# Kernel tuning notes

Hardware: AMD Instinct MI355X
Metric: run time of the kernel (lower is better)

## Reference

```python
import jax, jax.numpy as jnp
import numpy as np
import math

E = 2048        # embed_dim
H = 16          # num_heads
HD = E // H // 2  # head_dim = 64
DEPTH = 12
LAMBDA_INIT = 0.8 - 0.6 * math.exp(-0.3 * DEPTH)


def setup_inputs() -> dict:
    key = jax.random.key(0)
    ks = jax.random.split(key, 9)
    s = 0.02
    return {
        "x": jax.random.normal(ks[0], (2, 2048, E), jnp.float32),
        "Wq": jax.random.normal(ks[1], (E, E), jnp.float32) * s,
        "Wk": jax.random.normal(ks[2], (E, E), jnp.float32) * s,  # n_rep = 1
        "Wv": jax.random.normal(ks[3], (E, E), jnp.float32) * s,
        "Wo": jax.random.normal(ks[4], (E, E), jnp.float32) * s,
        "lq1": jax.random.normal(ks[5], (HD,), jnp.float32) * 0.1,
        "lk1": jax.random.normal(ks[6], (HD,), jnp.float32) * 0.1,
        "lq2": jax.random.normal(ks[7], (HD,), jnp.float32) * 0.1,
        "lk2": jax.random.normal(ks[8], (HD,), jnp.float32) * 0.1,
    }


def reference(x, Wq, Wk, Wv, Wo, lq1, lk1, lq2, lk2):
    b, t, e = x.shape
    scaling = HD ** (-0.5)
    # projections; split into 2*H sub-heads of dim HD for q/k, H heads of 2*HD for v
    q = (x @ Wq).reshape(b, t, 2 * H, HD).transpose(0, 2, 1, 3) * scaling  # [b,2H,t,hd]
    k = (x @ Wk).reshape(b, t, 2 * H, HD).transpose(0, 2, 1, 3)           # [b,2H,t,hd]
    v = (x @ Wv).reshape(b, t, H, 2 * HD).transpose(0, 2, 1, 3)           # [b,H,t,2hd]

    scores = jnp.einsum('bhqd,bhkd->bhqk', q, k)  # [b,2H,t,t]
    causal = jnp.triu(jnp.full((t, t), -jnp.inf, dtype=jnp.float32), 1)
    aw = jax.nn.softmax((scores + causal).astype(jnp.float32), axis=-1)

    lam = (jnp.exp(jnp.sum(lq1 * lk1)) - jnp.exp(jnp.sum(lq2 * lk2)) + LAMBDA_INIT)
    aw = aw.reshape(b, H, 2, t, t)
    aw = aw[:, :, 0] - lam * aw[:, :, 1]  # differential attention

    attn = jnp.einsum('bhqk,bhkd->bhqd', aw, v)  # [b,H,t,2hd]
    # RMSNorm over last dim (no affine), eps=1e-5
    attn = attn * jax.lax.rsqrt(jnp.mean(attn * attn, axis=-1, keepdims=True) + 1e-5)
    attn = attn * (1.0 - LAMBDA_INIT)
    attn = attn.transpose(0, 2, 1, 3).reshape(b, t, H * 2 * HD)
    return attn @ Wo
```

## Files before the change

### kernel.cpp

```cpp
#include <hip/hip_runtime.h>
#include <stdint.h>

typedef __bf16 bf16_t;
typedef __bf16 bf16x8 __attribute__((ext_vector_type(8)));
typedef __bf16 bf16x4 __attribute__((ext_vector_type(4)));
typedef float  f32x4  __attribute__((ext_vector_type(4)));
typedef float  f32x16 __attribute__((ext_vector_type(16)));
typedef unsigned int u32;

#define L2E 1.44269504088896340736f
#define LAMBDA_INIT 0.7836057665316245f
#define ONE_MINUS_LAMBDA_INIT 0.2163942334683755f

__device__ __forceinline__ void gload_lds16(const void* g, void* l) {
  __builtin_amdgcn_global_load_lds(
      (const __attribute__((address_space(1))) char*)(uintptr_t)g,
      (__attribute__((address_space(3))) char*)(uintptr_t)l, 16, 0, 0);
}

__device__ __forceinline__ f32x4 mfma_bf16(bf16x8 a, bf16x8 b, f32x4 c) {
  return __builtin_amdgcn_mfma_f32_16x16x32_bf16(a, b, c, 0, 0, 0);
}
__device__ __forceinline__ f32x16 mfma32(bf16x8 a, bf16x8 b, f32x16 c) {
  return __builtin_amdgcn_mfma_f32_32x32x16_bf16(a, b, c, 0, 0, 0);
}

__device__ __forceinline__ u32 pkbf(float a, float b) {
  union { bf16_t h[2]; u32 u; } x;
  x.h[0] = (bf16_t)a; x.h[1] = (bf16_t)b;
  return x.u;
}
__device__ __forceinline__ void pl32swap(u32& a, u32& b) {
  asm volatile("v_permlane32_swap_b32 %0, %1" : "+v"(a), "+v"(b));
}

__global__ __launch_bounds__(256) void cvt_bf16(const float* __restrict__ in,
                                                bf16_t* __restrict__ out) {
  const size_t idx = ((size_t)blockIdx.x * 256 + threadIdx.x) * 8;
  float4 a = *(const float4*)(in + idx);
  float4 c = *(const float4*)(in + idx + 4);
  bf16x8 v;
  v[0] = (bf16_t)a.x; v[1] = (bf16_t)a.y; v[2] = (bf16_t)a.z; v[3] = (bf16_t)a.w;
  v[4] = (bf16_t)c.x; v[5] = (bf16_t)c.y; v[6] = (bf16_t)c.z; v[7] = (bf16_t)c.w;
  *(bf16x8*)(out + idx) = v;
}

__global__ __launch_bounds__(256) void cvt_wT(const float* __restrict__ W,
                                              bf16_t* __restrict__ WT, float scale) {
  __shared__ float t[64][65];
  const int k0 = blockIdx.x * 64, n0 = blockIdx.y * 64;
  const int r = threadIdx.x >> 2, cg = threadIdx.x & 3;
#pragma unroll
  for (int q = 0; q < 4; ++q) {
    float4 v = *(const float4*)(W + (size_t)(k0 + r) * 2048 + n0 + cg * 16 + q * 4);
    t[r][cg * 16 + q * 4 + 0] = v.x;
    t[r][cg * 16 + q * 4 + 1] = v.y;
    t[r][cg * 16 + q * 4 + 2] = v.z;
    t[r][cg * 16 + q * 4 + 3] = v.w;
  }
  __syncthreads();
  bf16x8 o0, o1;
#pragma unroll
  for (int j = 0; j < 8; ++j) o0[j] = (bf16_t)(t[cg * 16 + j][r] * scale);
#pragma unroll
  for (int j = 0; j < 8; ++j) o1[j] = (bf16_t)(t[cg * 16 + 8 + j][r] * scale);
  bf16_t* dst = WT + (size_t)(n0 + r) * 2048 + k0 + cg * 16;
  *(bf16x8*)dst = o0;
  *(bf16x8*)(dst + 8) = o1;
}

__global__ void lam_kernel(const float* lq1, const float* lk1,
                           const float* lq2, const float* lk2, float* out) {
  const int l = threadIdx.x;
  float p1 = lq1[l] * lk1[l];
  float p2 = lq2[l] * lk2[l];
#pragma unroll
  for (int d = 1; d < 64; d <<= 1) {
    p1 += __shfl_xor(p1, d);
    p2 += __shfl_xor(p2, d);
  }
  if (l == 0) *out = expf(p1) - expf(p2) + LAMBDA_INIT;
}

template <int OUTMODE>
__global__ __launch_bounds__(256, 2) void gemm_bt(const bf16_t* __restrict__ A,
                                                  const bf16_t* __restrict__ Bt,
                                                  void* __restrict__ Cv) {
  __shared__ __align__(16) bf16_t As[128 * 64];
  __shared__ __align__(16) bf16_t Bs[128 * 64];
  const int tid = threadIdx.x;
  const int w = tid >> 6, lane = tid & 63;
  const int wr = w >> 1, wc = w & 1;
  const int lm = lane >> 4, ln = lane & 15;
  const int flat = (int)blockIdx.y * (int)gridDim.x + (int)blockIdx.x;
  const int swz = (flat & 7) * 64 + (flat >> 3);
  const int m0 = (swz & 31) * 128, n0 = (swz >> 5) * 128;

  const f32x4 vzero = {0.f, 0.f, 0.f, 0.f};
  f32x4 acc[4][4];
#pragma unroll
  for (int m = 0; m < 4; ++m)
#pragma unroll
    for (int n = 0; n < 4; ++n) acc[m][n] = vzero;

  for (int k0 = 0; k0 < 2048; k0 += 64) {
    __syncthreads();
#pragma unroll
    for (int j = 0; j < 4; ++j) {
      const int inst = w * 4 + j;
      const int row = inst * 8 + (lane >> 3);
      const int cb = ((lane & 7) * 16) ^ ((row & 7) << 4);
      gload_lds16(A + (size_t)(m0 + row) * 2048 + k0 + (cb >> 1),
                  (char*)As + inst * 1024);
      gload_lds16(Bt + (size_t)(n0 + row) * 2048 + k0 + (cb >> 1),
                  (char*)Bs + inst * 1024);
    }
    asm volatile("s_waitcnt vmcnt(0)" ::: "memory");
    __syncthreads();

#pragma unroll
    for (int kc = 0; kc < 2; ++kc) {
      bf16x8 af[4], bfr[4];
#pragma unroll
      for (int m = 0; m < 4; ++m) {
        const int row = wr * 64 + m * 16 + ln;
        int off = row * 128 + kc * 64 + lm * 16;
        off ^= (row & 7) << 4;
        af[m] = *(const bf16x8*)((const char*)As + off);
      }
#pragma unroll
      for (int n = 0; n < 4; ++n) {
        const int row = wc * 64 + n * 16 + ln;
        int off = row * 128 + kc * 64 + lm * 16;
        off ^= (row & 7) << 4;
        bfr[n] = *(const bf16x8*)((const char*)Bs + off);
      }
      __builtin_amdgcn_s_setprio(1);
#pragma unroll
      for (int m = 0; m < 4; ++m)
#pragma unroll
        for (int n = 0; n < 4; ++n) acc[m][n] = mfma_bf16(af[m], bfr[n], acc[m][n]);
      __builtin_amdgcn_s_setprio(0);
    }
  }

  if (OUTMODE == 0) {
    bf16_t* C = (bf16_t*)Cv;
#pragma unroll
    for (int m = 0; m < 4; ++m)
#pragma unroll
      for (int n = 0; n < 4; ++n)
#pragma unroll
        for (int r = 0; r < 4; ++r) {
          const size_t grow = m0 + wr * 64 + m * 16 + lm * 4 + r;
          const int gcol = n0 + wc * 64 + n * 16 + ln;
          C[grow * 2048 + gcol] = (bf16_t)acc[m][n][r];
        }
  } else if (OUTMODE == 1) {
    bf16_t* C = (bf16_t*)Cv;
#pragma unroll
    for (int m = 0; m < 4; ++m)
#pragma unroll
      for (int n = 0; n < 4; ++n) {
        const size_t gcol = n0 + wc * 64 + n * 16 + ln;
        const int growb = m0 + wr * 64 + m * 16 + lm * 4;
        bf16x4 v;
#pragma unroll
        for (int r = 0; r < 4; ++r) v[r] = (bf16_t)acc[m][n][r];
        *(bf16x4*)(C + gcol * 4096 + growb) = v;
      }
  } else {
    float* C = (float*)Cv;
#pragma unroll
    for (int m = 0; m < 4; ++m)
#pragma unroll
      for (int n = 0; n < 4; ++n)
#pragma unroll
        for (int r = 0; r < 4; ++r) {
          const size_t grow = m0 + wr * 64 + m * 16 + lm * 4 + r;
          const int gcol = n0 + wc * 64 + n * 16 + ln;
          C[grow * 2048 + gcol] = acc[m][n][r];
        }
  }
}

__global__ __launch_bounds__(256, 2) void flash_diff(const bf16_t* __restrict__ Q,
                                                     const bf16_t* __restrict__ K,
                                                     const bf16_t* __restrict__ Vt,
                                                     bf16_t* __restrict__ attnb,
                                                     const float* __restrict__ lamP) {
  __shared__ __align__(16) char smem[81920];

  const int tid = threadIdx.x;
  const int w = tid >> 6, lane = tid & 63;
  const int qh = w >> 1, s = w & 1;
  const int l31 = lane & 31, hi = lane >> 5;
  const int h = blockIdx.y, b = blockIdx.z;
  const size_t bt0 = (size_t)b * 2048;
  const float lam = *lamP;

  auto stage_kv = [&](int buf, int k0) {
#pragma unroll
    for (int j = 0; j < 4; ++j) {
      const int inst = w * 4 + j;
      {
        const int row = inst * 4 + (lane >> 4);
        const int cb = ((lane & 15) * 16) ^ ((row & 7) << 4);
        gload_lds16(K + (bt0 + k0 + row) * 2048 + h * 128 + (cb >> 1),
                    smem + 16384 + buf * 16384 + inst * 1024);
      }
      {
        const int row = inst * 8 + (lane >> 3);
        const int cb = ((lane & 7) * 16) ^ ((row & 7) << 4);
        gload_lds16(Vt + (size_t)(h * 128 + row) * 4096 + bt0 + k0 + (cb >> 1),
                    smem + 49152 + buf * 16384 + inst * 1024);
      }
    }
  };

  for (int half = 0; half < 2; ++half) {
    const int qt = half == 0 ? (int)blockIdx.x : 31 - (int)blockIdx.x;
    const int q0 = qt * 64;
    const int qloc = qh * 32 + l31;

#pragma unroll
    for (int j = 0; j < 4; ++j) {
      const int inst = w * 4 + j;
      const int row = inst * 4 + (lane >> 4);
      const int cb = ((lane & 15) * 16) ^ ((row & 7) << 4);
      gload_lds16(Q + (bt0 + q0 + row) * 2048 + h * 128 + (cb >> 1),
                  smem + inst * 1024);
    }
    stage_kv(0, 0);
    asm volatile("s_waitcnt vmcnt(0)" ::: "memory");
    __syncthreads();

    bf16x8 qf[4];
#pragma unroll
    for (int kc = 0; kc < 4; ++kc) {
      const int row = qloc;
      int off = row * 256 + s * 128 + kc * 32 + hi * 16;
      off ^= (row & 7) << 4;
      qf[kc] = *(const bf16x8*)((const char*)smem + off);
    }

    f32x16 accv[4];
#pragma unroll
    for (int m = 0; m < 4; ++m)
#pragma unroll
      for (int r = 0; r < 16; ++r) accv[m][r] = 0.f;
    float lsum = 0.f;

    int cur = 0;
    for (int kt = 0; kt <= qt; ++kt) {
      if (kt < qt) stage_kv(cur ^ 1, (kt + 1) * 64);

      const char* Ksb = (const char*)smem + 16384 + cur * 16384;
      const char* Vsb = (const char*)smem + 49152 + cur * 16384;

      f32x16 sa[2];
#pragma unroll
      for (int m = 0; m < 2; ++m)
#pragma unroll
        for (int r = 0; r < 16; ++r) sa[m][r] = 0.f;
      __builtin_amdgcn_s_setprio(1);
#pragma unroll
      for (int kc = 0; kc < 4; ++kc) {
#pragma unroll
        for (int mt = 0; mt < 2; ++mt) {
          const int row = mt * 32 + l31;
          int off = row * 256 + s * 128 + kc * 32 + hi * 16;
          off ^= (row & 7) << 4;
          bf16x8 kf = *(const bf16x8*)(Ksb + off);
          sa[mt] = mfma32(kf, qf[kc], sa[mt]);
        }
      }
      __builtin_amdgcn_s_setprio(0);

      if (kt == qt) {
#pragma unroll
        for (int mt = 0; mt < 2; ++mt)
#pragma unroll
          for (int r = 0; r < 16; ++r) {
            const int key = mt * 32 + (r & 3) + 8 * (r >> 2) + 4 * hi;
            if (key > qloc) sa[mt][r] = -1e30f;
          }
      }

      bf16x8 pf[2][2];
#pragma unroll
      for (int mt = 0; mt < 2; ++mt) {
        float p[16];
#pragma unroll
        for (int r = 0; r < 16; ++r) {
          p[r] = exp2f(sa[mt][r]);
          lsum += p[r];
        }
        u32 c0 = pkbf(p[0], p[1]),   c1 = pkbf(p[2], p[3]);
        u32 c2 = pkbf(p[4], p[5]),   c3 = pkbf(p[6], p[7]);
        u32 c4 = pkbf(p[8], p[9]),   c5 = pkbf(p[10], p[11]);
        u32 c6 = pkbf(p[12], p[13]), c7 = pkbf(p[14], p[15]);
        pl32swap(c0, c2); pl32swap(c1, c3);
        pl32swap(c4, c6); pl32swap(c5, c7);
        union { u32 u[4]; bf16x8 v; } f0, f1;
        f0.u[0] = c0; f0.u[1] = c1; f0.u[2] = c2; f0.u[3] = c3;
        f1.u[0] = c4; f1.u[1] = c5; f1.u[2] = c6; f1.u[3] = c7;
        pf[mt][0] = f0.v;
        pf[mt][1] = f1.v;
      }

      __builtin_amdgcn_s_setprio(1);
#pragma unroll
      for (int mt4 = 0; mt4 < 4; ++mt4) {
        const int row = mt4 * 32 + l31;
        const int rswz = (row & 7) << 4;
#pragma unroll
        for (int st = 0; st < 4; ++st) {
          int off = row * 128 + st * 32 + hi * 16;
          off ^= rswz;
          bf16x8 vf = *(const bf16x8*)(Vsb + off);
          accv[mt4] = mfma32(vf, pf[st >> 1][st & 1], accv[mt4]);
        }
      }
      __builtin_amdgcn_s_setprio(0);

      asm volatile("s_waitcnt vmcnt(0)" ::: "memory");
      __syncthreads();
      cur ^= 1;
    }

    lsum += __shfl_xor(lsum, 32);
    const float rl = 1.0f / lsum;
    float* Obuf = (float*)(smem + 16384);

    if (s == 1) {
#pragma unroll
      for (int mt4 = 0; mt4 < 4; ++mt4)
#pragma unroll
        for (int q2 = 0; q2 < 4; ++q2) {
          f32x4 v;
#pragma unroll
          for (int e = 0; e < 4; ++e) v[e] = accv[mt4][q2 * 4 + e] * rl;
          const int d = mt4 * 32 + q2 * 8 + hi * 4;
          *(f32x4*)(Obuf + (size_t)qloc * 128 + d) = v;
        }
    }
    __syncthreads();
    if (s == 0) {
      float o[4][16];
      float ss = 0.f;
#pragma unroll
      for (int mt4 = 0; mt4 < 4; ++mt4)
#pragma unroll
        for (int q2 = 0; q2 < 4; ++q2) {
          const int d = mt4 * 32 + q2 * 8 + hi * 4;
          f32x4 ov = *(const f32x4*)(Obuf + (size_t)qloc * 128 + d);
#pragma unroll
          for (int e = 0; e < 4; ++e) {
            const float v = accv[mt4][q2 * 4 + e] * rl - lam * ov[e];
            o[mt4][q2 * 4 + e] = v;
            ss += v * v;
          }
        }
      ss += __shfl_xor(ss, 32);
      const float sc = rsqrtf(ss * (1.0f / 128.f) + 1e-5f) * ONE_MINUS_LAMBDA_INIT;
      const size_t grow = bt0 + q0 + qloc;
#pragma unroll
      for (int mt4 = 0; mt4 < 4; ++mt4)
#pragma unroll
        for (int q2 = 0; q2 < 4; ++q2) {
          const int d = mt4 * 32 + q2 * 8 + hi * 4;
          bf16x4 v;
#pragma unroll
          for (int e = 0; e < 4; ++e) v[e] = (bf16_t)(o[mt4][q2 * 4 + e] * sc);
          *(bf16x4*)(attnb + grow * 2048 + h * 128 + d) = v;
        }
    }
    __syncthreads();
  }
}

extern "C" void kernel_launch(void* const* d_in, const int* in_sizes, int n_in,
                              void* d_out, int out_size, void* d_ws, size_t ws_size,
                              hipStream_t stream) {
  const float* x   = (const float*)d_in[0];
  const float* Wq  = (const float*)d_in[1];
  const float* Wk  = (const float*)d_in[2];
  const float* Wv  = (const float*)d_in[3];
  const float* Wo  = (const float*)d_in[4];
  const float* lq1 = (const float*)d_in[5];
  const float* lk1 = (const float*)d_in[6];
  const float* lq2 = (const float*)d_in[7];
  const float* lk2 = (const float*)d_in[8];

  char* ws = (char*)d_ws;
  bf16_t* xb    = (bf16_t*)(ws + 0);
  bf16_t* wqT   = (bf16_t*)(ws + 16777216);
  bf16_t* wkT   = (bf16_t*)(ws + 25165824);
  bf16_t* wvT   = (bf16_t*)(ws + 33554432);
  bf16_t* woT   = (bf16_t*)(ws + 41943040);
  bf16_t* Qb    = (bf16_t*)(ws + 50331648);
  bf16_t* Kb    = (bf16_t*)(ws + 67108864);
  bf16_t* Vtb   = (bf16_t*)(ws + 16777216);
  bf16_t* attnb = (bf16_t*)(ws + 0);
  float*  lamP  = (float*)(ws + 83886080);

  cvt_bf16<<<4096, 256, 0, stream>>>(x, xb);
  cvt_wT<<<dim3(32, 32), 256, 0, stream>>>(Wq, wqT, 0.125f * L2E);
  cvt_wT<<<dim3(32, 32), 256, 0, stream>>>(Wk, wkT, 1.0f);
  cvt_wT<<<dim3(32, 32), 256, 0, stream>>>(Wv, wvT, 1.0f);
  cvt_wT<<<dim3(32, 32), 256, 0, stream>>>(Wo, woT, 1.0f);
  lam_kernel<<<1, 64, 0, stream>>>(lq1, lk1, lq2, lk2, lamP);

  gemm_bt<0><<<dim3(32, 16), 256, 0, stream>>>(xb, wqT, (void*)Qb);
  gemm_bt<0><<<dim3(32, 16), 256, 0, stream>>>(xb, wkT, (void*)Kb);
  gemm_bt<1><<<dim3(32, 16), 256, 0, stream>>>(xb, wvT, (void*)Vtb);

  flash_diff<<<dim3(16, 16, 2), 256, 0, stream>>>(Qb, Kb, Vtb, attnb, lamP);

  gemm_bt<2><<<dim3(32, 16), 256, 0, stream>>>(attnb, woT, d_out);
}
```

Before: 288.5 us.

## Load Q and V directly to registers, shrink LDS, remap blocks per XCD

The attention kernel now loads Q fragments and V tiles straight from global memory into registers, and only K goes through double-buffered LDS. LDS use drops from 80KB to 32KB, and launch bounds rise to 3 blocks per CU for more occupancy. The grid is flattened to 1D and remapped so each XCD handles a fixed set of (batch, head) pairs, which should improve L2 reuse of K/V. The K swizzle also widens to 16 rows. The tradeoffs are uncoalesced, higher-latency V reads from global memory inside the inner loop and more register pressure.

New measurement: 347.5 us. +20.5%, slower.

```diff
diff --git a/kernel.cpp b/kernel.cpp
--- a/kernel.cpp
+++ b/kernel.cpp
@@ -184,66 +184,52 @@
   }
 }
 
-__global__ __launch_bounds__(256, 2) void flash_diff(const bf16_t* __restrict__ Q,
+__global__ __launch_bounds__(256, 3) void flash_diff(const bf16_t* __restrict__ Q,
                                                      const bf16_t* __restrict__ K,
                                                      const bf16_t* __restrict__ Vt,
                                                      bf16_t* __restrict__ attnb,
                                                      const float* __restrict__ lamP) {
-  __shared__ __align__(16) char smem[81920];
+  __shared__ __align__(16) char smem[32768];
 
   const int tid = threadIdx.x;
   const int w = tid >> 6, lane = tid & 63;
   const int qh = w >> 1, s = w & 1;
   const int l31 = lane & 31, hi = lane >> 5;
-  const int h = blockIdx.y, b = blockIdx.z;
+
+  const int bid = (int)blockIdx.x;
+  const int xcd = bid & 7, p = bid >> 3;
+  const int qtp = p & 15, g = p >> 4;
+  const int hb = g * 8 + xcd;
+  const int h = hb & 15, b = hb >> 4;
   const size_t bt0 = (size_t)b * 2048;
   const float lam = *lamP;
 
-  auto stage_kv = [&](int buf, int k0) {
-#pragma unroll
-    for (int j = 0; j < 4; ++j) {
-      const int inst = w * 4 + j;
-      {
-        const int row = inst * 4 + (lane >> 4);
-        const int cb = ((lane & 15) * 16) ^ ((row & 7) << 4);
-        gload_lds16(K + (bt0 + k0 + row) * 2048 + h * 128 + (cb >> 1),
-                    smem + 16384 + buf * 16384 + inst * 1024);
-      }
-      {
-        const int row = inst * 8 + (lane >> 3);
-        const int cb = ((lane & 7) * 16) ^ ((row & 7) << 4);
-        gload_lds16(Vt + (size_t)(h * 128 + row) * 4096 + bt0 + k0 + (cb >> 1),
-                    smem + 49152 + buf * 16384 + inst * 1024);
-      }
-    }
-  };
-
-  for (int half = 0; half < 2; ++half) {
-    const int qt = half == 0 ? (int)blockIdx.x : 31 - (int)blockIdx.x;
-    const int q0 = qt * 64;
-    const int qloc = qh * 32 + l31;
-
+  auto stage_k = [&](int buf, int k0) {
 #pragma unroll
     for (int j = 0; j < 4; ++j) {
       const int inst = w * 4 + j;
       const int row = inst * 4 + (lane >> 4);
-      const int cb = ((lane & 15) * 16) ^ ((row & 7) << 4);
-      gload_lds16(Q + (bt0 + q0 + row) * 2048 + h * 128 + (cb >> 1),
-                  smem + inst * 1024);
-    }
-    stage_kv(0, 0);
+      const int cb = ((lane & 15) * 16) ^ ((row & 15) << 4);
+      gload_lds16(K + (bt0 + k0 + row) * 2048 + h * 128 + (cb >> 1),
+                  smem + buf * 16384 + inst * 1024);
+    }
+  };
+
+  for (int half = 0; half < 2; ++half) {
+    const int qt = half == 0 ? qtp : 31 - qtp;
+    const int q0 = qt * 64;
+    const int qloc = qh * 32 + l31;
+
+    bf16x8 qf[4];
+#pragma unroll
+    for (int kc = 0; kc < 4; ++kc)
+      qf[kc] = *(const bf16x8*)(Q + (bt0 + q0 + qloc) * 2048 + h * 128 +
+                                s * 64 + kc * 16 + hi * 8);
+
+    stage_k(0, 0);
     asm volatile("s_waitcnt vmcnt(0)" ::: "memory");
     __syncthreads();
 
-    bf16x8 qf[4];
-#pragma unroll
-    for (int kc = 0; kc < 4; ++kc) {
-      const int row = qloc;
-      int off = row * 256 + s * 128 + kc * 32 + hi * 16;
-      off ^= (row & 7) << 4;
-      qf[kc] = *(const bf16x8*)((const char*)smem + off);
-    }
-
     f32x16 accv[4];
 #pragma unroll
     for (int m = 0; m < 4; ++m)
@@ -253,53 +239,52 @@
 
     int cur = 0;
     for (int kt = 0; kt <= qt; ++kt) {
-      if (kt < qt) stage_kv(cur ^ 1, (kt + 1) * 64);
-
-      const char* Ksb = (const char*)smem + 16384 + cur * 16384;
-      const char* Vsb = (const char*)smem + 49152 + cur * 16384;
-
-      f32x16 sa[2];
-#pragma unroll
-      for (int m = 0; m < 2; ++m)
-#pragma unroll
-        for (int r = 0; r < 16; ++r) sa[m][r] = 0.f;
-      __builtin_amdgcn_s_setprio(1);
-#pragma unroll
-      for (int kc = 0; kc < 4; ++kc) {
-#pragma unroll
-        for (int mt = 0; mt < 2; ++mt) {
-          const int row = mt * 32 + l31;
+      if (kt < qt) stage_k(cur ^ 1, (kt + 1) * 64);
+
+      const bf16_t* vbase =
+          Vt + (size_t)(h * 128 + l31) * 4096 + bt0 + kt * 64 + hi * 8;
+      bf16x8 vf[2][4];
+#pragma unroll
+      for (int kk = 0; kk < 4; ++kk)
+        vf[0][kk] = *(const bf16x8*)(vbase + kk * 16);
+
+      const char* Ksb = (const char*)smem + cur * 16384;
+
+      bf16x8 pf[2][2];
+#pragma unroll
+      for (int mt = 0; mt < 2; ++mt) {
+        f32x16 sa;
+#pragma unroll
+        for (int r = 0; r < 16; ++r) sa[r] = 0.f;
+        const int row = mt * 32 + l31;
+        const int rswz = (row & 15) << 4;
+        __builtin_amdgcn_s_setprio(1);
+#pragma unroll
+        for (int kc = 0; kc < 4; ++kc) {
           int off = row * 256 + s * 128 + kc * 32 + hi * 16;
-          off ^= (row & 7) << 4;
+          off ^= rswz;
           bf16x8 kf = *(const bf16x8*)(Ksb + off);
-          sa[mt] = mfma32(kf, qf[kc], sa[mt]);
-        }
-      }
-      __builtin_amdgcn_s_setprio(0);
-
-      if (kt == qt) {
-#pragma unroll
-        for (int mt = 0; mt < 2; ++mt)
+          sa = mfma32(kf, qf[kc], sa);
+        }
+        __builtin_amdgcn_s_setprio(0);
+
+        if (kt == qt) {
 #pragma unroll
           for (int r = 0; r < 16; ++r) {
             const int key = mt * 32 + (r & 3) + 8 * (r >> 2) + 4 * hi;
-            if (key > qloc) sa[mt][r] = -1e30f;
+            if (key > qloc) sa[r] = -1e30f;
           }
-      }
-
-      bf16x8 pf[2][2];
-#pragma unroll
-      for (int mt = 0; mt < 2; ++mt) {
-        float p[16];
+        }
+        float pv[16];
 #pragma unroll
         for (int r = 0; r < 16; ++r) {
-          p[r] = exp2f(sa[mt][r]);
-          lsum += p[r];
-        }
-        u32 c0 = pkbf(p[0], p[1]),   c1 = pkbf(p[2], p[3]);
-        u32 c2 = pkbf(p[4], p[5]),   c3 = pkbf(p[6], p[7]);
-        u32 c4 = pkbf(p[8], p[9]),   c5 = pkbf(p[10], p[11]);
-        u32 c6 = pkbf(p[12], p[13]), c7 = pkbf(p[14], p[15]);
+          pv[r] = exp2f(sa[r]);
+          lsum += pv[r];
+        }
+        u32 c0 = pkbf(pv[0], pv[1]),   c1 = pkbf(pv[2], pv[3]);
+        u32 c2 = pkbf(pv[4], pv[5]),   c3 = pkbf(pv[6], pv[7]);
+        u32 c4 = pkbf(pv[8], pv[9]),   c5 = pkbf(pv[10], pv[11]);
+        u32 c6 = pkbf(pv[12], pv[13]), c7 = pkbf(pv[14], pv[15]);
         pl32swap(c0, c2); pl32swap(c1, c3);
         pl32swap(c4, c6); pl32swap(c5, c7);
         union { u32 u[4]; bf16x8 v; } f0, f1;
@@ -309,20 +294,20 @@
         pf[mt][1] = f1.v;
       }
 
-      __builtin_amdgcn_s_setprio(1);
-#pragma unroll
-      for (int mt4 = 0; mt4 < 4; ++mt4) {
-        const int row = mt4 * 32 + l31;
-        const int rswz = (row & 7) << 4;
-#pragma unroll
-        for (int st = 0; st < 4; ++st) {
-          int off = row * 128 + st * 32 + hi * 16;
-          off ^= rswz;
-          bf16x8 vf = *(const bf16x8*)(Vsb + off);
-          accv[mt4] = mfma32(vf, pf[st >> 1][st & 1], accv[mt4]);
-        }
+#pragma unroll
+      for (int gdx = 0; gdx < 4; ++gdx) {
+        if (gdx < 3) {
+          const bf16_t* nb = vbase + (size_t)(gdx + 1) * 32 * 4096;
+#pragma unroll
+          for (int kk = 0; kk < 4; ++kk)
+            vf[(gdx + 1) & 1][kk] = *(const bf16x8*)(nb + kk * 16);
+        }
+        __builtin_amdgcn_s_setprio(1);
+#pragma unroll
+        for (int kk = 0; kk < 4; ++kk)
+          accv[gdx] = mfma32(vf[gdx & 1][kk], pf[kk >> 1][kk & 1], accv[gdx]);
+        __builtin_amdgcn_s_setprio(0);
       }
-      __builtin_amdgcn_s_setprio(0);
 
       asm volatile("s_waitcnt vmcnt(0)" ::: "memory");
       __syncthreads();
@@ -331,7 +316,7 @@
 
     lsum += __shfl_xor(lsum, 32);
     const float rl = 1.0f / lsum;
-    float* Obuf = (float*)(smem + 16384);
+    float* Obuf = (float*)smem;
 
     if (s == 1) {
 #pragma unroll
@@ -416,7 +401,7 @@
   gemm_bt<0><<<dim3(32, 16), 256, 0, stream>>>(xb, wkT, (void*)Kb);
   gemm_bt<1><<<dim3(32, 16), 256, 0, stream>>>(xb, wvT, (void*)Vtb);
 
-  flash_diff<<<dim3(16, 16, 2), 256, 0, stream>>>(Qb, Kb, Vtb, attnb, lamP);
+  flash_diff<<<512, 256, 0, stream>>>(Qb, Kb, Vtb, attnb, lamP);
 
   gemm_bt<2><<<dim3(32, 16), 256, 0, stream>>>(attnb, woT, d_out);
 }
```
